# Kernel tuning notes

Measured on AMD Instinct MI355X. Metric: run time of the kernel, lower is better.

Reference implementation:

```python
import jax, jax.numpy as jnp
import numpy as np

N_NODES = 50000
N_EDGES = 1600000
IN_FEAT = 128
OUT_FEAT = 32
N_HEADS = 4
NEG_SLOPE = 0.2


def setup_inputs() -> dict:
    key = jax.random.key(0)
    ks = jax.random.split(key, 7)
    h = jax.random.normal(ks[0], (N_NODES, IN_FEAT), dtype=jnp.float32)
    W = jax.random.normal(ks[1], (IN_FEAT, N_HEADS * OUT_FEAT), dtype=jnp.float32) * 0.05
    attn_l = jax.random.normal(ks[2], (N_HEADS, OUT_FEAT), dtype=jnp.float32) * 0.1
    attn_r = jax.random.normal(ks[3], (N_HEADS, OUT_FEAT), dtype=jnp.float32) * 0.1
    bias = jax.random.normal(ks[4], (N_HEADS * OUT_FEAT,), dtype=jnp.float32) * 0.01
    src = jax.random.randint(ks[5], (N_EDGES,), 0, N_NODES, dtype=jnp.int32)
    dst = jax.random.randint(ks[6], (N_EDGES,), 0, N_NODES, dtype=jnp.int32)
    return {"h": h, "W": W, "attn_l": attn_l, "attn_r": attn_r, "bias": bias, "src": src, "dst": dst}


def reference(h, W, attn_l, attn_r, bias, src, dst):
    N = h.shape[0]
    H, F = attn_l.shape
    # linear projection, [N, H, F]
    feat = (h @ W).reshape(N, H, F)
    # per-node attention halves
    el = jnp.einsum('nhf,hf->nh', feat, attn_l)  # [N, H]
    er = jnp.einsum('nhf,hf->nh', feat, attn_r)  # [N, H]
    # edge scores: e_ij = leaky_relu(el[src] + er[dst])
    e = jax.nn.leaky_relu(el[src] + er[dst], negative_slope=NEG_SLOPE)  # [E, H]
    # edge softmax over incoming edges of each dst node (numerically stable)
    m = jax.ops.segment_max(e, dst, num_segments=N)  # [N, H]
    m = jnp.where(jnp.isfinite(m), m, jnp.zeros_like(m))  # zero-in-degree guard
    ex = jnp.exp(e - m[dst])  # [E, H]
    denom = jax.ops.segment_sum(ex, dst, num_segments=N)  # [N, H]
    alpha = ex / jnp.maximum(denom[dst], 1e-9)  # [E, H]
    # weighted scatter-sum aggregation
    msg = feat[src] * alpha[:, :, None]  # [E, H, F]
    rst = jax.ops.segment_sum(msg, dst, num_segments=N)  # [N, H, F]
    rst = rst + bias.reshape(1, H, F)
    rst = jax.nn.relu(rst)
    # wrapper: norm=None, dropout=0.0 (eval), mean over heads
    return jnp.mean(rst, axis=1)  # [N, F]
```

## Files before the change

kernel.cpp:

```cpp
#include <hip/hip_runtime.h>
#include <hip/hip_bf16.h>
#include <hip/hip_fp16.h>
#include <math.h>


#define NEG_SLOPE 0.2f
#define HEADS 4
#define FEAT_OUT 32
#define FEAT_ALL 128
#define IN_FEAT 128
#define KP 136
#define NBLK1 512
#define NBKT_MAX 512
#define CHE_MAX 3200
#define CHB_MAX 6144

typedef _Float16 half8 __attribute__((ext_vector_type(8)));
typedef float float4v __attribute__((ext_vector_type(4)));
typedef unsigned int uint4v __attribute__((ext_vector_type(4)));

__device__ __forceinline__ float leaky(float v) {
    return v > 0.f ? v : NEG_SLOPE * v;
}

__global__ __launch_bounds__(256) void k1_fused(
    const int* __restrict__ src, const int* __restrict__ dst, int E,
    int che, int nbkt,
    unsigned int* __restrict__ ds, int* __restrict__ hist,
    const float* __restrict__ h, const float* __restrict__ W,
    const float* __restrict__ attn_l, const float* __restrict__ attn_r,
    unsigned char* __restrict__ feat8, float2* __restrict__ elsc,
    float* __restrict__ er, int N, int nG) {
    __shared__ _Float16 sf[64 * KP];
    const int t = threadIdx.x;

    if ((int)blockIdx.x >= nG) {
        const int blk = blockIdx.x - nG;
        int* hb = (int*)sf;
        for (int i = t; i < nbkt; i += 256) hb[i] = 0;
        __syncthreads();
        const int e_lo = blk * che;
        int e_hi = e_lo + che; if (e_hi > E) e_hi = E;
        for (int e0 = e_lo + t * 4; e0 < e_hi; e0 += 1024) {
            if (e0 + 3 < e_hi) {
                uint4v s4 = *(const uint4v*)(src + e0);
                uint4v d4 = *(const uint4v*)(dst + e0);
                uint4v r;
#pragma unroll
                for (int j = 0; j < 4; j++) r[j] = (s4[j] << 16) | d4[j];
                *(uint4v*)(ds + e0) = r;
#pragma unroll
                for (int j = 0; j < 4; j++) atomicAdd(&hb[d4[j] >> 7], 1);
            } else {
                for (int e = e0; e < e_hi; ++e) {
                    unsigned s = (unsigned)src[e], d = (unsigned)dst[e];
                    ds[e] = (s << 16) | d;
                    atomicAdd(&hb[d >> 7], 1);
                }
            }
        }
        __syncthreads();
        for (int i = t; i < nbkt; i += 256) hist[i * NBLK1 + blk] = hb[i];
        return;
    }

    const int n0 = blockIdx.x * 64;
    const int wv_ = t >> 6;
    const int lane = t & 63;
    const int m16 = lane & 15;
    const int quad = lane >> 4;
    const int rowA = wv_ * 16 + m16;
    int nA = n0 + rowA; if (nA > N - 1) nA = N - 1;
    const float* hp = h + (size_t)nA * IN_FEAT + quad * 8;

    float4v acc[8];
#pragma unroll
    for (int i = 0; i < 8; i++) acc[i] = (float4v){0.f, 0.f, 0.f, 0.f};

#pragma unroll
    for (int k0 = 0; k0 < 128; k0 += 32) {
        float4 a0 = *(const float4*)(hp + k0);
        float4 a1 = *(const float4*)(hp + k0 + 4);
        half8 a;
        a[0] = (_Float16)a0.x; a[1] = (_Float16)a0.y;
        a[2] = (_Float16)a0.z; a[3] = (_Float16)a0.w;
        a[4] = (_Float16)a1.x; a[5] = (_Float16)a1.y;
        a[6] = (_Float16)a1.z; a[7] = (_Float16)a1.w;
        const float* wp = W + (size_t)(k0 + quad * 8) * FEAT_ALL + m16;
#pragma unroll
        for (int tN = 0; tN < 8; tN++) {
            const float* wpt = wp + tN * 16;
            half8 b;
            b[0] = (_Float16)wpt[0];
            b[1] = (_Float16)wpt[FEAT_ALL];
            b[2] = (_Float16)wpt[2 * FEAT_ALL];
            b[3] = (_Float16)wpt[3 * FEAT_ALL];
            b[4] = (_Float16)wpt[4 * FEAT_ALL];
            b[5] = (_Float16)wpt[5 * FEAT_ALL];
            b[6] = (_Float16)wpt[6 * FEAT_ALL];
            b[7] = (_Float16)wpt[7 * FEAT_ALL];
            acc[tN] = __builtin_amdgcn_mfma_f32_16x16x32_f16(a, b, acc[tN], 0, 0, 0);
        }
    }

#pragma unroll
    for (int tN = 0; tN < 8; tN++)
#pragma unroll
        for (int r = 0; r < 4; r++) {
            int row = wv_ * 16 + quad * 4 + r;
            sf[row * KP + tN * 16 + m16] = (_Float16)acc[tN][r];
        }
    __syncthreads();

    {
        int r = t >> 2, hh = t & 3;
        int n = n0 + r;
        if (n < N) {
            const _Float16* sp_ = &sf[r * KP + hh * FEAT_OUT];
            float sl = 0.f, sr = 0.f, mx = 0.f;
#pragma unroll
            for (int f = 0; f < FEAT_OUT; f++) {
                float v = (float)sp_[f];
                sl += v * attn_l[hh * FEAT_OUT + f];
                sr += v * attn_r[hh * FEAT_OUT + f];
                mx = fmaxf(mx, fabsf(v));
            }
            er[n * HEADS + hh] = sr;
            elsc[n * HEADS + hh] = make_float2(sl, mx * (1.f / 127.f));
            const float inv = mx > 0.f ? 127.f / mx : 0.f;
            unsigned int w[8];
#pragma unroll
            for (int k2 = 0; k2 < 8; k2++) {
                unsigned int wv = 0;
#pragma unroll
                for (int j = 0; j < 4; j++) {
                    float v = (float)sp_[k2 * 4 + j];
                    int q = __float2int_rn(v * inv);
                    wv |= ((unsigned int)(q & 0xff)) << (8 * j);
                }
                w[k2] = wv;
            }
            uint4* dp = (uint4*)(feat8 + (size_t)n * FEAT_ALL + hh * 32);
            dp[0] = make_uint4(w[0], w[1], w[2], w[3]);
            dp[1] = make_uint4(w[4], w[5], w[6], w[7]);
        }
    }
}

__global__ __launch_bounds__(256) void s1_scan(
    const int* __restrict__ hist, int* __restrict__ base1,
    int* __restrict__ tot, int nbkt) {
    __shared__ int sm[256];
    const int b = blockIdx.x;
    const int t = threadIdx.x;
    const int v0 = hist[b * NBLK1 + 2 * t];
    const int v1 = hist[b * NBLK1 + 2 * t + 1];
    const int s = v0 + v1;
    sm[t] = s; __syncthreads();
    for (int off = 1; off < 256; off <<= 1) {
        int x = (t >= off) ? sm[t - off] : 0;
        __syncthreads();
        sm[t] += x;
        __syncthreads();
    }
    const int excl = sm[t] - s;
    base1[(2 * t) * nbkt + b] = excl;
    base1[(2 * t + 1) * nbkt + b] = excl + v0;
    if (t == 255) tot[b] = sm[255];
}

__global__ __launch_bounds__(256) void s2_scan(
    const int* __restrict__ tot, int* __restrict__ bb, int nbkt) {
    __shared__ int sm[256];
    const int t = threadIdx.x;
    const int v0 = (2 * t < nbkt) ? tot[2 * t] : 0;
    const int v1 = (2 * t + 1 < nbkt) ? tot[2 * t + 1] : 0;
    const int s = v0 + v1;
    sm[t] = s; __syncthreads();
    for (int off = 1; off < 256; off <<= 1) {
        int x = (t >= off) ? sm[t - off] : 0;
        __syncthreads();
        sm[t] += x;
        __syncthreads();
    }
    const int excl = sm[t] - s;
    if (2 * t <= nbkt) bb[2 * t] = excl;
    if (2 * t + 1 <= nbkt) bb[2 * t + 1] = excl + v0;
}

__global__ __launch_bounds__(256) void p2_place(
    const unsigned int* __restrict__ ds, const int* __restrict__ hist,
    const int* __restrict__ base1, const int* __restrict__ bb,
    unsigned int* __restrict__ srt, int E, int che, int nbkt) {
    __shared__ int cur[NBKT_MAX];
    __shared__ int l0[NBKT_MAX];
    __shared__ int gst[NBKT_MAX];
    __shared__ int sm[256];
    __shared__ unsigned int stage[CHE_MAX];
    __shared__ int gaddr[CHE_MAX];
    const int t = threadIdx.x;
    const int blk = blockIdx.x;
    const int e_lo = blk * che;
    int e_hi = e_lo + che; if (e_hi > E) e_hi = E;
    int cnt = e_hi - e_lo; if (cnt < 0) cnt = 0;

    if (che <= CHE_MAX) {
        const int b0 = 2 * t, b1 = 2 * t + 1;
        const int h0 = (b0 < nbkt) ? hist[b0 * NBLK1 + blk] : 0;
        const int h1 = (b1 < nbkt) ? hist[b1 * NBLK1 + blk] : 0;
        const int s = h0 + h1;
        sm[t] = s; __syncthreads();
        for (int off = 1; off < 256; off <<= 1) {
            int x = (t >= off) ? sm[t - off] : 0;
            __syncthreads();
            sm[t] += x;
            __syncthreads();
        }
        const int excl = sm[t] - s;
        if (b0 < nbkt) {
            l0[b0] = excl; cur[b0] = excl;
            gst[b0] = bb[b0] + base1[blk * nbkt + b0] - excl;
        }
        if (b1 < nbkt) {
            l0[b1] = excl + h0; cur[b1] = excl + h0;
            gst[b1] = bb[b1] + base1[blk * nbkt + b1] - (excl + h0);
        }
        __syncthreads();
        for (int e0 = e_lo + t * 4; e0 < e_hi; e0 += 1024) {
            if (e0 + 3 < e_hi) {
                uint4v q = *(const uint4v*)(ds + e0);
#pragma unroll
                for (int j = 0; j < 4; j++) {
                    int b = (int)(q[j] & 0xffffu) >> 7;
                    int r = atomicAdd(&cur[b], 1);
                    stage[r] = q[j];
                    gaddr[r] = gst[b] + r;
                }
            } else {
                for (int e = e0; e < e_hi; ++e) {
                    unsigned q = ds[e];
                    int b = (int)(q & 0xffffu) >> 7;
                    int r = atomicAdd(&cur[b], 1);
                    stage[r] = q;
                    gaddr[r] = gst[b] + r;
                }
            }
        }
        __syncthreads();
        for (int i = t; i < cnt; i += 256)
            srt[gaddr[i]] = stage[i];
    } else {
        for (int i = t; i < nbkt; i += 256)
            cur[i] = bb[i] + base1[blk * nbkt + i];
        __syncthreads();
        for (int e0 = e_lo + t * 4; e0 < e_hi; e0 += 1024) {
            for (int e = e0; e < e_hi && e < e0 + 4; ++e) {
                unsigned q = ds[e];
                int b = (int)(q & 0xffffu) >> 7;
                int idx = atomicAdd(&cur[b], 1);
                srt[idx] = q;
            }
        }
    }
}

__global__ __launch_bounds__(256) void p3_bucket(
    const unsigned int* __restrict__ srt, const int* __restrict__ bb,
    unsigned short* __restrict__ slots16, unsigned int* __restrict__ rpd,
    int N) {
    __shared__ int h2[128];
    __shared__ int nbuf[128];
    __shared__ unsigned short stage16[CHB_MAX];
    const int b = blockIdx.x;
    const int t = threadIdx.x;
    const int s0 = bb[b];
    const int M = bb[b + 1] - s0;
    const int lo = b << 7;
    if (t < 128) h2[t] = 0;
    __syncthreads();
    for (int i = t; i < M; i += 256) {
        unsigned q = srt[s0 + i];
        atomicAdd(&h2[(int)(q & 0xffffu) - lo], 1);
    }
    __syncthreads();
    int hv = 0;
    if (t < 128) hv = h2[t];
    for (int off = 1; off < 128; off <<= 1) {
        int x = 0;
        if (t < 128 && t >= off) x = h2[t - off];
        __syncthreads();
        if (t < 128) h2[t] += x;
        __syncthreads();
    }
    if (t < 128) {
        const int excl = h2[t] - hv;
        nbuf[t] = excl;
        const int n = lo + t;
        if (n < N) {
            int dg = hv > 255 ? 255 : hv;
            rpd[n] = ((unsigned)(s0 + excl) << 8) | (unsigned)dg;
        }
    }
    __syncthreads();
    if (t < 128) h2[t] = nbuf[t];
    __syncthreads();
    if (M <= CHB_MAX) {
        for (int i = t; i < M; i += 256) {
            unsigned q = srt[s0 + i];
            int n7 = (int)(q & 0xffffu) - lo;
            int r = atomicAdd(&h2[n7], 1);
            stage16[r] = (unsigned short)(q >> 16);
        }
        __syncthreads();
        for (int i = t; i < M; i += 256)
            slots16[s0 + i] = stage16[i];
    } else {
        for (int i = t; i < M; i += 256) {
            unsigned q = srt[s0 + i];
            int n7 = (int)(q & 0xffffu) - lo;
            int r = atomicAdd(&h2[n7], 1);
            slots16[s0 + r] = (unsigned short)(q >> 16);
        }
    }
}

__global__ __launch_bounds__(256) void k5_node(
    const unsigned int* __restrict__ rpd, const unsigned short* __restrict__ slots16,
    const float2* __restrict__ elsc, const float* __restrict__ er,
    const unsigned char* __restrict__ feat8, const float* __restrict__ bias,
    float* __restrict__ out, int N) {
    const int lane = threadIdx.x & 63;
    const int p = blockIdx.x & 7;
    const int g = blockIdx.x >> 3;
    const int NPER = (N + 7) >> 3;
    const int hi = ((p + 1) * NPER < N) ? (p + 1) * NPER : N;
    const int n = p * NPER + g * 4 + (threadIdx.x >> 6);
    if (n >= hi) return;
    const unsigned rd = rpd[n];
    const int deg = (int)(rd & 0xffu);
    const unsigned short* sp = slots16 + (rd >> 8);

    const int sub4 = lane >> 4;
    const int q4 = lane & 15;
    const int hh = q4 >> 2;
    const float ernh = er[n * HEADS + hh];

    float acc[8];
#pragma unroll
    for (int j = 0; j < 8; j++) acc[j] = 0.f;
    float den = 0.f;

#pragma unroll 4
    for (int i = sub4; i < deg; i += 4) {
        int s = (int)sp[i];
        float2 es = elsc[s * HEADS + hh];
        float ex = __expf(leaky(es.x + ernh));
        uint2 u = *(const uint2*)(feat8 + (size_t)s * FEAT_ALL + q4 * 8);
        float exs = ex * es.y;
        den += ex;
        union { uint2 v; signed char b[8]; } cv;
        cv.v = u;
        acc[0] += exs * (float)cv.b[0];
        acc[1] += exs * (float)cv.b[1];
        acc[2] += exs * (float)cv.b[2];
        acc[3] += exs * (float)cv.b[3];
        acc[4] += exs * (float)cv.b[4];
        acc[5] += exs * (float)cv.b[5];
        acc[6] += exs * (float)cv.b[6];
        acc[7] += exs * (float)cv.b[7];
    }

#pragma unroll
    for (int j = 0; j < 8; j++) {
        acc[j] += __shfl_xor(acc[j], 16);
        acc[j] += __shfl_xor(acc[j], 32);
    }
    den += __shfl_xor(den, 16);
    den += __shfl_xor(den, 32);
    const float idh = 1.f / fmaxf(den, 1e-9f);

    const float4 b0 = ((const float4*)bias)[q4 * 2];
    const float4 b1 = ((const float4*)bias)[q4 * 2 + 1];
    float v[8];
    v[0] = fmaxf(acc[0] * idh + b0.x, 0.f); v[1] = fmaxf(acc[1] * idh + b0.y, 0.f);
    v[2] = fmaxf(acc[2] * idh + b0.z, 0.f); v[3] = fmaxf(acc[3] * idh + b0.w, 0.f);
    v[4] = fmaxf(acc[4] * idh + b1.x, 0.f); v[5] = fmaxf(acc[5] * idh + b1.y, 0.f);
    v[6] = fmaxf(acc[6] * idh + b1.z, 0.f); v[7] = fmaxf(acc[7] * idh + b1.w, 0.f);
#pragma unroll
    for (int j = 0; j < 8; j++) {
        v[j] += __shfl_xor(v[j], 4);
        v[j] += __shfl_xor(v[j], 8);
    }
    if (lane < 4) {
        float4 o0 = make_float4(v[0] * 0.25f, v[1] * 0.25f, v[2] * 0.25f, v[3] * 0.25f);
        float4 o1 = make_float4(v[4] * 0.25f, v[5] * 0.25f, v[6] * 0.25f, v[7] * 0.25f);
        float* op = out + (size_t)n * FEAT_OUT + lane * 8;
        ((float4*)op)[0] = o0;
        ((float4*)op)[1] = o1;
    }
}

extern "C" void kernel_launch(void* const* d_in, const int* in_sizes, int n_in,
                              void* d_out, int out_size, void* d_ws, size_t ws_size,
                              hipStream_t stream) {
    const float* h      = (const float*)d_in[0];
    const float* W      = (const float*)d_in[1];
    const float* attn_l = (const float*)d_in[2];
    const float* attn_r = (const float*)d_in[3];
    const float* bias   = (const float*)d_in[4];
    const int*   src    = (const int*)d_in[5];
    const int*   dst    = (const int*)d_in[6];
    float* out = (float*)d_out;

    const int N = in_sizes[0] / IN_FEAT;
    const int E = in_sizes[5];
    const int nbkt = (N + 127) >> 7;
    const int che = (((E + NBLK1 - 1) / NBLK1) + 3) & ~3;

    char* w = (char*)d_ws;
    auto alloc = [&](size_t bytes) { char* r = w; w += (bytes + 255) & ~(size_t)255; return r; };
    unsigned char* feat8   = (unsigned char*)alloc((size_t)N * FEAT_ALL);
    float2*        elsc    = (float2*)alloc((size_t)N * HEADS * sizeof(float2));
    float*         er      = (float*)alloc((size_t)N * HEADS * sizeof(float));
    unsigned int*  rpd     = (unsigned int*)alloc((size_t)N * 4);
    unsigned int*  ds      = (unsigned int*)alloc((size_t)E * 4);
    unsigned int*  srt     = (unsigned int*)alloc((size_t)E * 4);
    unsigned short* slots16 = (unsigned short*)alloc((size_t)E * 2);
    int*           hist    = (int*)alloc((size_t)NBLK1 * nbkt * 4);
    int*           base1   = (int*)alloc((size_t)NBLK1 * nbkt * 4);
    int*           tot     = (int*)alloc((size_t)nbkt * 4);
    int*           bb      = (int*)alloc((size_t)(nbkt + 1) * 4);

    const int nG = (N + 63) / 64;
    k1_fused<<<nG + NBLK1, 256, 0, stream>>>(src, dst, E, che, nbkt, ds, hist,
                                             h, W, attn_l, attn_r,
                                             feat8, elsc, er, N, nG);
    s1_scan<<<nbkt, 256, 0, stream>>>(hist, base1, tot, nbkt);
    s2_scan<<<1, 256, 0, stream>>>(tot, bb, nbkt);
    p2_place<<<NBLK1, 256, 0, stream>>>(ds, hist, base1, bb, srt, E, che, nbkt);
    p3_bucket<<<nbkt, 256, 0, stream>>>(srt, bb, slots16, rpd, N);

    const int NPER = (N + 7) >> 3;
    const int nb5 = 8 * ((NPER + 3) / 4);
    k5_node<<<nb5, 256, 0, stream>>>(rpd, slots16, elsc, er, feat8, bias, out, N);
}
```

Measured before the change: 177.6 us.

## Merge scan, place and bucket kernels into one cooperative kernel with grid syncs

Replaces four separate launches (two scans, global placement, per-bucket sort) with a single cooperative kernel of 512 blocks that separates the phases with grid.sync(). Shared memory is overlaid through a union so one block can serve every phase. The aim is to remove per-launch overhead and the gaps between dependent small kernels. In exchange, grid-wide barriers are costly, all 512 blocks must be co-resident, and phases that use only nbkt blocks leave the rest idle.

```diff
diff --git a/kernel.cpp b/kernel.cpp
--- a/kernel.cpp
+++ b/kernel.cpp
@@ -1,4 +1,5 @@
 #include <hip/hip_runtime.h>
+#include <hip/hip_cooperative_groups.h>
 #include <hip/hip_bf16.h>
 #include <hip/hip_fp16.h>
 #include <math.h>
@@ -14,6 +15,8 @@
 #define NBKT_MAX 512
 #define CHE_MAX 3200
 #define CHB_MAX 6144
+
+namespace cg = cooperative_groups;
 
 typedef _Float16 half8 __attribute__((ext_vector_type(8)));
 typedef float float4v __attribute__((ext_vector_type(4)));
@@ -147,179 +150,172 @@
     }
 }
 
-__global__ __launch_bounds__(256) void s1_scan(
-    const int* __restrict__ hist, int* __restrict__ base1,
-    int* __restrict__ tot, int nbkt) {
-    __shared__ int sm[256];
-    const int b = blockIdx.x;
-    const int t = threadIdx.x;
-    const int v0 = hist[b * NBLK1 + 2 * t];
-    const int v1 = hist[b * NBLK1 + 2 * t + 1];
-    const int s = v0 + v1;
-    sm[t] = s; __syncthreads();
-    for (int off = 1; off < 256; off <<= 1) {
-        int x = (t >= off) ? sm[t - off] : 0;
-        __syncthreads();
-        sm[t] += x;
-        __syncthreads();
-    }
-    const int excl = sm[t] - s;
-    base1[(2 * t) * nbkt + b] = excl;
-    base1[(2 * t + 1) * nbkt + b] = excl + v0;
-    if (t == 255) tot[b] = sm[255];
-}
-
-__global__ __launch_bounds__(256) void s2_scan(
-    const int* __restrict__ tot, int* __restrict__ bb, int nbkt) {
-    __shared__ int sm[256];
-    const int t = threadIdx.x;
-    const int v0 = (2 * t < nbkt) ? tot[2 * t] : 0;
-    const int v1 = (2 * t + 1 < nbkt) ? tot[2 * t + 1] : 0;
-    const int s = v0 + v1;
-    sm[t] = s; __syncthreads();
-    for (int off = 1; off < 256; off <<= 1) {
-        int x = (t >= off) ? sm[t - off] : 0;
-        __syncthreads();
-        sm[t] += x;
-        __syncthreads();
-    }
-    const int excl = sm[t] - s;
-    if (2 * t <= nbkt) bb[2 * t] = excl;
-    if (2 * t + 1 <= nbkt) bb[2 * t + 1] = excl + v0;
-}
-
-__global__ __launch_bounds__(256) void p2_place(
+__global__ __launch_bounds__(256) void ksort(
     const unsigned int* __restrict__ ds, const int* __restrict__ hist,
-    const int* __restrict__ base1, const int* __restrict__ bb,
-    unsigned int* __restrict__ srt, int E, int che, int nbkt) {
-    __shared__ int cur[NBKT_MAX];
-    __shared__ int l0[NBKT_MAX];
-    __shared__ int gst[NBKT_MAX];
-    __shared__ int sm[256];
-    __shared__ unsigned int stage[CHE_MAX];
-    __shared__ int gaddr[CHE_MAX];
+    int* __restrict__ base1, int* __restrict__ bb, int* __restrict__ tot,
+    unsigned int* __restrict__ srt, unsigned short* __restrict__ slots16,
+    unsigned int* __restrict__ rpd, int E, int che, int nbkt, int N) {
+    __shared__ union {
+        struct { int sm[256]; } a;
+        struct {
+            int cur[NBKT_MAX]; int gst[NBKT_MAX]; int sm[256];
+            unsigned int stage[CHE_MAX]; int gaddr[CHE_MAX];
+        } c;
+        struct { int h2[128]; int nbuf[128]; unsigned short stage16[CHB_MAX]; } d;
+    } u;
     const int t = threadIdx.x;
     const int blk = blockIdx.x;
-    const int e_lo = blk * che;
-    int e_hi = e_lo + che; if (e_hi > E) e_hi = E;
-    int cnt = e_hi - e_lo; if (cnt < 0) cnt = 0;
-
-    if (che <= CHE_MAX) {
-        const int b0 = 2 * t, b1 = 2 * t + 1;
-        const int h0 = (b0 < nbkt) ? hist[b0 * NBLK1 + blk] : 0;
-        const int h1 = (b1 < nbkt) ? hist[b1 * NBLK1 + blk] : 0;
-        const int s = h0 + h1;
-        sm[t] = s; __syncthreads();
+    cg::grid_group grid = cg::this_grid();
+
+    if (blk < nbkt) {
+        const int b = blk;
+        const int v0 = hist[b * NBLK1 + 2 * t];
+        const int v1 = hist[b * NBLK1 + 2 * t + 1];
+        const int s = v0 + v1;
+        u.a.sm[t] = s; __syncthreads();
         for (int off = 1; off < 256; off <<= 1) {
-            int x = (t >= off) ? sm[t - off] : 0;
-            __syncthreads();
-            sm[t] += x;
-            __syncthreads();
-        }
-        const int excl = sm[t] - s;
-        if (b0 < nbkt) {
-            l0[b0] = excl; cur[b0] = excl;
-            gst[b0] = bb[b0] + base1[blk * nbkt + b0] - excl;
-        }
-        if (b1 < nbkt) {
-            l0[b1] = excl + h0; cur[b1] = excl + h0;
-            gst[b1] = bb[b1] + base1[blk * nbkt + b1] - (excl + h0);
-        }
-        __syncthreads();
-        for (int e0 = e_lo + t * 4; e0 < e_hi; e0 += 1024) {
-            if (e0 + 3 < e_hi) {
-                uint4v q = *(const uint4v*)(ds + e0);
-#pragma unroll
-                for (int j = 0; j < 4; j++) {
-                    int b = (int)(q[j] & 0xffffu) >> 7;
-                    int r = atomicAdd(&cur[b], 1);
-                    stage[r] = q[j];
-                    gaddr[r] = gst[b] + r;
+            int x = (t >= off) ? u.a.sm[t - off] : 0;
+            __syncthreads();
+            u.a.sm[t] += x;
+            __syncthreads();
+        }
+        const int excl = u.a.sm[t] - s;
+        base1[(2 * t) * nbkt + b] = excl;
+        base1[(2 * t + 1) * nbkt + b] = excl + v0;
+        if (t == 255) tot[b] = u.a.sm[255];
+    }
+    grid.sync();
+
+    if (blk == 0) {
+        const int v0 = (2 * t < nbkt) ? tot[2 * t] : 0;
+        const int v1 = (2 * t + 1 < nbkt) ? tot[2 * t + 1] : 0;
+        const int s = v0 + v1;
+        u.a.sm[t] = s; __syncthreads();
+        for (int off = 1; off < 256; off <<= 1) {
+            int x = (t >= off) ? u.a.sm[t - off] : 0;
+            __syncthreads();
+            u.a.sm[t] += x;
+            __syncthreads();
+        }
+        const int excl = u.a.sm[t] - s;
+        if (2 * t <= nbkt) bb[2 * t] = excl;
+        if (2 * t + 1 <= nbkt) bb[2 * t + 1] = excl + v0;
+    }
+    grid.sync();
+
+    {
+        const int e_lo = blk * che;
+        int e_hi = e_lo + che; if (e_hi > E) e_hi = E;
+        int cnt = e_hi - e_lo; if (cnt < 0) cnt = 0;
+        if (che <= CHE_MAX) {
+            const int b0 = 2 * t, b1 = 2 * t + 1;
+            const int h0 = (b0 < nbkt) ? hist[b0 * NBLK1 + blk] : 0;
+            const int h1 = (b1 < nbkt) ? hist[b1 * NBLK1 + blk] : 0;
+            const int s = h0 + h1;
+            u.c.sm[t] = s; __syncthreads();
+            for (int off = 1; off < 256; off <<= 1) {
+                int x = (t >= off) ? u.c.sm[t - off] : 0;
+                __syncthreads();
+                u.c.sm[t] += x;
+                __syncthreads();
+            }
+            const int excl = u.c.sm[t] - s;
+            if (b0 < nbkt) {
+                u.c.cur[b0] = excl;
+                u.c.gst[b0] = bb[b0] + base1[blk * nbkt + b0] - excl;
+            }
+            if (b1 < nbkt) {
+                u.c.cur[b1] = excl + h0;
+                u.c.gst[b1] = bb[b1] + base1[blk * nbkt + b1] - (excl + h0);
+            }
+            __syncthreads();
+            for (int e0 = e_lo + t * 4; e0 < e_hi; e0 += 1024) {
+                if (e0 + 3 < e_hi) {
+                    uint4v q = *(const uint4v*)(ds + e0);
+#pragma unroll
+                    for (int j = 0; j < 4; j++) {
+                        int b = (int)(q[j] & 0xffffu) >> 7;
+                        int r = atomicAdd(&u.c.cur[b], 1);
+                        u.c.stage[r] = q[j];
+                        u.c.gaddr[r] = u.c.gst[b] + r;
+                    }
+                } else {
+                    for (int e = e0; e < e_hi; ++e) {
+                        unsigned q = ds[e];
+                        int b = (int)(q & 0xffffu) >> 7;
+                        int r = atomicAdd(&u.c.cur[b], 1);
+                        u.c.stage[r] = q;
+                        u.c.gaddr[r] = u.c.gst[b] + r;
+                    }
                 }
-            } else {
-                for (int e = e0; e < e_hi; ++e) {
-                    unsigned q = ds[e];
-                    int b = (int)(q & 0xffffu) >> 7;
-                    int r = atomicAdd(&cur[b], 1);
-                    stage[r] = q;
-                    gaddr[r] = gst[b] + r;
-                }
-            }
-        }
-        __syncthreads();
-        for (int i = t; i < cnt; i += 256)
-            srt[gaddr[i]] = stage[i];
-    } else {
-        for (int i = t; i < nbkt; i += 256)
-            cur[i] = bb[i] + base1[blk * nbkt + i];
-        __syncthreads();
-        for (int e0 = e_lo + t * 4; e0 < e_hi; e0 += 1024) {
-            for (int e = e0; e < e_hi && e < e0 + 4; ++e) {
+            }
+            __syncthreads();
+            for (int i = t; i < cnt; i += 256)
+                srt[u.c.gaddr[i]] = u.c.stage[i];
+        } else {
+            for (int i = t; i < nbkt; i += 256)
+                u.c.cur[i] = bb[i] + base1[blk * nbkt + i];
+            __syncthreads();
+            for (int e = e_lo + t; e < e_hi; e += 256) {
                 unsigned q = ds[e];
                 int b = (int)(q & 0xffffu) >> 7;
-                int idx = atomicAdd(&cur[b], 1);
+                int idx = atomicAdd(&u.c.cur[b], 1);
                 srt[idx] = q;
             }
         }
     }
-}
-
-__global__ __launch_bounds__(256) void p3_bucket(
-    const unsigned int* __restrict__ srt, const int* __restrict__ bb,
-    unsigned short* __restrict__ slots16, unsigned int* __restrict__ rpd,
-    int N) {
-    __shared__ int h2[128];
-    __shared__ int nbuf[128];
-    __shared__ unsigned short stage16[CHB_MAX];
-    const int b = blockIdx.x;
-    const int t = threadIdx.x;
-    const int s0 = bb[b];
-    const int M = bb[b + 1] - s0;
-    const int lo = b << 7;
-    if (t < 128) h2[t] = 0;
-    __syncthreads();
-    for (int i = t; i < M; i += 256) {
-        unsigned q = srt[s0 + i];
-        atomicAdd(&h2[(int)(q & 0xffffu) - lo], 1);
-    }
-    __syncthreads();
-    int hv = 0;
-    if (t < 128) hv = h2[t];
-    for (int off = 1; off < 128; off <<= 1) {
-        int x = 0;
-        if (t < 128 && t >= off) x = h2[t - off];
-        __syncthreads();
-        if (t < 128) h2[t] += x;
-        __syncthreads();
-    }
-    if (t < 128) {
-        const int excl = h2[t] - hv;
-        nbuf[t] = excl;
-        const int n = lo + t;
-        if (n < N) {
-            int dg = hv > 255 ? 255 : hv;
-            rpd[n] = ((unsigned)(s0 + excl) << 8) | (unsigned)dg;
-        }
-    }
-    __syncthreads();
-    if (t < 128) h2[t] = nbuf[t];
-    __syncthreads();
-    if (M <= CHB_MAX) {
+    grid.sync();
+
+    if (blk < nbkt) {
+        const int b = blk;
+        const int s0 = bb[b];
+        const int M = bb[b + 1] - s0;
+        const int lo = b << 7;
+        if (t < 128) u.d.h2[t] = 0;
+        __syncthreads();
         for (int i = t; i < M; i += 256) {
             unsigned q = srt[s0 + i];
-            int n7 = (int)(q & 0xffffu) - lo;
-            int r = atomicAdd(&h2[n7], 1);
-            stage16[r] = (unsigned short)(q >> 16);
-        }
-        __syncthreads();
-        for (int i = t; i < M; i += 256)
-            slots16[s0 + i] = stage16[i];
-    } else {
-        for (int i = t; i < M; i += 256) {
-            unsigned q = srt[s0 + i];
-            int n7 = (int)(q & 0xffffu) - lo;
-            int r = atomicAdd(&h2[n7], 1);
-            slots16[s0 + r] = (unsigned short)(q >> 16);
+            atomicAdd(&u.d.h2[(int)(q & 0xffffu) - lo], 1);
+        }
+        __syncthreads();
+        int hv = 0;
+        if (t < 128) hv = u.d.h2[t];
+        for (int off = 1; off < 128; off <<= 1) {
+            int x = 0;
+            if (t < 128 && t >= off) x = u.d.h2[t - off];
+            __syncthreads();
+            if (t < 128) u.d.h2[t] += x;
+            __syncthreads();
+        }
+        if (t < 128) {
+            const int excl = u.d.h2[t] - hv;
+            u.d.nbuf[t] = excl;
+            const int n = lo + t;
+            if (n < N) {
+                int dg = hv > 255 ? 255 : hv;
+                rpd[n] = ((unsigned)(s0 + excl) << 8) | (unsigned)dg;
+            }
+        }
+        __syncthreads();
+        if (t < 128) u.d.h2[t] = u.d.nbuf[t];
+        __syncthreads();
+        if (M <= CHB_MAX) {
+            for (int i = t; i < M; i += 256) {
+                unsigned q = srt[s0 + i];
+                int n7 = (int)(q & 0xffffu) - lo;
+                int r = atomicAdd(&u.d.h2[n7], 1);
+                u.d.stage16[r] = (unsigned short)(q >> 16);
+            }
+            __syncthreads();
+            for (int i = t; i < M; i += 256)
+                slots16[s0 + i] = u.d.stage16[i];
+        } else {
+            for (int i = t; i < M; i += 256) {
+                unsigned q = srt[s0 + i];
+                int n7 = (int)(q & 0xffffu) - lo;
+                int r = atomicAdd(&u.d.h2[n7], 1);
+                slots16[s0 + r] = (unsigned short)(q >> 16);
+            }
         }
     }
 }
@@ -413,9 +409,9 @@
     float* out = (float*)d_out;
 
     const int N = in_sizes[0] / IN_FEAT;
-    const int E = in_sizes[5];
-    const int nbkt = (N + 127) >> 7;
-    const int che = (((E + NBLK1 - 1) / NBLK1) + 3) & ~3;
+    int E = in_sizes[5];
+    int nbkt = (N + 127) >> 7;
+    int che = (((E + NBLK1 - 1) / NBLK1) + 3) & ~3;
 
     char* w = (char*)d_ws;
     auto alloc = [&](size_t bytes) { char* r = w; w += (bytes + 255) & ~(size_t)255; return r; };
@@ -430,15 +426,17 @@
     int*           base1   = (int*)alloc((size_t)NBLK1 * nbkt * 4);
     int*           tot     = (int*)alloc((size_t)nbkt * 4);
     int*           bb      = (int*)alloc((size_t)(nbkt + 1) * 4);
+    int N_ = N;
 
     const int nG = (N + 63) / 64;
     k1_fused<<<nG + NBLK1, 256, 0, stream>>>(src, dst, E, che, nbkt, ds, hist,
                                              h, W, attn_l, attn_r,
                                              feat8, elsc, er, N, nG);
-    s1_scan<<<nbkt, 256, 0, stream>>>(hist, base1, tot, nbkt);
-    s2_scan<<<1, 256, 0, stream>>>(tot, bb, nbkt);
-    p2_place<<<NBLK1, 256, 0, stream>>>(ds, hist, base1, bb, srt, E, che, nbkt);
-    p3_bucket<<<nbkt, 256, 0, stream>>>(srt, bb, slots16, rpd, N);
+
+    void* args[] = {(void*)&ds, (void*)&hist, (void*)&base1, (void*)&bb,
+                    (void*)&tot, (void*)&srt, (void*)&slots16, (void*)&rpd,
+                    (void*)&E, (void*)&che, (void*)&nbkt, (void*)&N_};
+    hipLaunchCooperativeKernel((void*)ksort, dim3(NBLK1), dim3(256), args, 0, stream);
 
     const int NPER = (N + 7) >> 3;
     const int nb5 = 8 * ((NPER + 3) / 4);
```

After: 385.3 us. 117% more time.

## Fuse bucket-level sort into aggregation kernel and fold total scan into placement

Applied to the files above, without the earlier changes.

Removes the separate total-scan kernel by having every p2_place block redundantly scan the bucket totals in shared memory. Removes the p3_bucket kernel and the rpd/slots16 buffers: the aggregation kernel now handles a quarter-bucket of 32 nodes per block, counting-sorts that quarter's edges into shared memory, and aggregates straight from there. This cuts two launches and one global write/read pass over the edges. In exchange, each bucket's edge list is scanned four times (once per quarter), each block recomputes its start offset with a reduction, and there is a slow fallback path when a quarter holds more than the staging capacity.

```diff
diff --git a/kernel.cpp b/kernel.cpp
--- a/kernel.cpp
+++ b/kernel.cpp
@@ -13,7 +13,7 @@
 #define NBLK1 512
 #define NBKT_MAX 512
 #define CHE_MAX 3200
-#define CHB_MAX 6144
+#define QCAP 2048
 
 typedef _Float16 half8 __attribute__((ext_vector_type(8)));
 typedef float float4v __attribute__((ext_vector_type(4)));
@@ -169,32 +169,13 @@
     if (t == 255) tot[b] = sm[255];
 }
 
-__global__ __launch_bounds__(256) void s2_scan(
-    const int* __restrict__ tot, int* __restrict__ bb, int nbkt) {
-    __shared__ int sm[256];
-    const int t = threadIdx.x;
-    const int v0 = (2 * t < nbkt) ? tot[2 * t] : 0;
-    const int v1 = (2 * t + 1 < nbkt) ? tot[2 * t + 1] : 0;
-    const int s = v0 + v1;
-    sm[t] = s; __syncthreads();
-    for (int off = 1; off < 256; off <<= 1) {
-        int x = (t >= off) ? sm[t - off] : 0;
-        __syncthreads();
-        sm[t] += x;
-        __syncthreads();
-    }
-    const int excl = sm[t] - s;
-    if (2 * t <= nbkt) bb[2 * t] = excl;
-    if (2 * t + 1 <= nbkt) bb[2 * t + 1] = excl + v0;
-}
-
 __global__ __launch_bounds__(256) void p2_place(
     const unsigned int* __restrict__ ds, const int* __restrict__ hist,
-    const int* __restrict__ base1, const int* __restrict__ bb,
+    const int* __restrict__ base1, const int* __restrict__ tot,
     unsigned int* __restrict__ srt, int E, int che, int nbkt) {
     __shared__ int cur[NBKT_MAX];
-    __shared__ int l0[NBKT_MAX];
     __shared__ int gst[NBKT_MAX];
+    __shared__ int bbloc[NBKT_MAX];
     __shared__ int sm[256];
     __shared__ unsigned int stage[CHE_MAX];
     __shared__ int gaddr[CHE_MAX];
@@ -203,6 +184,23 @@
     const int e_lo = blk * che;
     int e_hi = e_lo + che; if (e_hi > E) e_hi = E;
     int cnt = e_hi - e_lo; if (cnt < 0) cnt = 0;
+
+    {
+        const int v0 = (2 * t < nbkt) ? tot[2 * t] : 0;
+        const int v1 = (2 * t + 1 < nbkt) ? tot[2 * t + 1] : 0;
+        const int s = v0 + v1;
+        sm[t] = s; __syncthreads();
+        for (int off = 1; off < 256; off <<= 1) {
+            int x = (t >= off) ? sm[t - off] : 0;
+            __syncthreads();
+            sm[t] += x;
+            __syncthreads();
+        }
+        const int excl = sm[t] - s;
+        if (2 * t < nbkt) bbloc[2 * t] = excl;
+        if (2 * t + 1 < nbkt) bbloc[2 * t + 1] = excl + v0;
+    }
+    __syncthreads();
 
     if (che <= CHE_MAX) {
         const int b0 = 2 * t, b1 = 2 * t + 1;
@@ -218,12 +216,12 @@
         }
         const int excl = sm[t] - s;
         if (b0 < nbkt) {
-            l0[b0] = excl; cur[b0] = excl;
-            gst[b0] = bb[b0] + base1[blk * nbkt + b0] - excl;
+            cur[b0] = excl;
+            gst[b0] = bbloc[b0] + base1[blk * nbkt + b0] - excl;
         }
         if (b1 < nbkt) {
-            l0[b1] = excl + h0; cur[b1] = excl + h0;
-            gst[b1] = bb[b1] + base1[blk * nbkt + b1] - (excl + h0);
+            cur[b1] = excl + h0;
+            gst[b1] = bbloc[b1] + base1[blk * nbkt + b1] - (excl + h0);
         }
         __syncthreads();
         for (int e0 = e_lo + t * 4; e0 < e_hi; e0 += 1024) {
@@ -251,152 +249,164 @@
             srt[gaddr[i]] = stage[i];
     } else {
         for (int i = t; i < nbkt; i += 256)
-            cur[i] = bb[i] + base1[blk * nbkt + i];
-        __syncthreads();
-        for (int e0 = e_lo + t * 4; e0 < e_hi; e0 += 1024) {
-            for (int e = e0; e < e_hi && e < e0 + 4; ++e) {
-                unsigned q = ds[e];
-                int b = (int)(q & 0xffffu) >> 7;
-                int idx = atomicAdd(&cur[b], 1);
-                srt[idx] = q;
-            }
-        }
-    }
-}
-
-__global__ __launch_bounds__(256) void p3_bucket(
-    const unsigned int* __restrict__ srt, const int* __restrict__ bb,
-    unsigned short* __restrict__ slots16, unsigned int* __restrict__ rpd,
-    int N) {
-    __shared__ int h2[128];
-    __shared__ int nbuf[128];
-    __shared__ unsigned short stage16[CHB_MAX];
-    const int b = blockIdx.x;
+            cur[i] = bbloc[i] + base1[blk * nbkt + i];
+        __syncthreads();
+        for (int e = e_lo + t; e < e_hi; e += 256) {
+            unsigned q = ds[e];
+            int b = (int)(q & 0xffffu) >> 7;
+            int idx = atomicAdd(&cur[b], 1);
+            srt[idx] = q;
+        }
+    }
+}
+
+__global__ __launch_bounds__(256) void k5_bkt(
+    const unsigned int* __restrict__ srt, const int* __restrict__ tot,
+    const float2* __restrict__ elsc, const float* __restrict__ er,
+    const unsigned char* __restrict__ feat8, const float* __restrict__ bias,
+    float* __restrict__ out, int N, int nbkt) {
+    __shared__ int red[256];
+    __shared__ int rowptr[33];
+    __shared__ int curq[32];
+    __shared__ unsigned short stage16[QCAP];
     const int t = threadIdx.x;
-    const int s0 = bb[b];
-    const int M = bb[b + 1] - s0;
-    const int lo = b << 7;
-    if (t < 128) h2[t] = 0;
+    const int p = blockIdx.x & 7;
+    const int kk_ = blockIdx.x >> 3;
+    const int b = (kk_ >> 2) * 8 + p;
+    const int qtr = kk_ & 3;
+    if (b >= nbkt) return;
+
+    int partial = 0;
+    for (int i = t; i < b; i += 256) partial += tot[i];
+    red[t] = partial; __syncthreads();
+    for (int off = 128; off > 0; off >>= 1) {
+        if (t < off) red[t] += red[t + off];
+        __syncthreads();
+    }
+    const int s0 = red[0];
+    const int M = tot[b];
+    const int lo = (b << 7) + qtr * 32;
+
+    if (t < 32) curq[t] = 0;
     __syncthreads();
     for (int i = t; i < M; i += 256) {
-        unsigned q = srt[s0 + i];
-        atomicAdd(&h2[(int)(q & 0xffffu) - lo], 1);
+        int u = (int)(srt[s0 + i] & 0xffffu) - lo;
+        if ((unsigned)u < 32u) atomicAdd(&curq[u], 1);
     }
     __syncthreads();
-    int hv = 0;
-    if (t < 128) hv = h2[t];
-    for (int off = 1; off < 128; off <<= 1) {
-        int x = 0;
-        if (t < 128 && t >= off) x = h2[t - off];
-        __syncthreads();
-        if (t < 128) h2[t] += x;
-        __syncthreads();
-    }
-    if (t < 128) {
-        const int excl = h2[t] - hv;
-        nbuf[t] = excl;
-        const int n = lo + t;
-        if (n < N) {
-            int dg = hv > 255 ? 255 : hv;
-            rpd[n] = ((unsigned)(s0 + excl) << 8) | (unsigned)dg;
-        }
+    if (t == 0) {
+        int acc = 0;
+#pragma unroll
+        for (int j = 0; j < 32; j++) { rowptr[j] = acc; acc += curq[j]; }
+        rowptr[32] = acc;
     }
     __syncthreads();
-    if (t < 128) h2[t] = nbuf[t];
-    __syncthreads();
-    if (M <= CHB_MAX) {
+    const int Mq = rowptr[32];
+    const bool staged = (Mq <= QCAP);
+    if (staged) {
+        if (t < 32) curq[t] = rowptr[t];
+        __syncthreads();
         for (int i = t; i < M; i += 256) {
             unsigned q = srt[s0 + i];
-            int n7 = (int)(q & 0xffffu) - lo;
-            int r = atomicAdd(&h2[n7], 1);
-            stage16[r] = (unsigned short)(q >> 16);
-        }
-        __syncthreads();
-        for (int i = t; i < M; i += 256)
-            slots16[s0 + i] = stage16[i];
-    } else {
-        for (int i = t; i < M; i += 256) {
-            unsigned q = srt[s0 + i];
-            int n7 = (int)(q & 0xffffu) - lo;
-            int r = atomicAdd(&h2[n7], 1);
-            slots16[s0 + r] = (unsigned short)(q >> 16);
-        }
-    }
-}
-
-__global__ __launch_bounds__(256) void k5_node(
-    const unsigned int* __restrict__ rpd, const unsigned short* __restrict__ slots16,
-    const float2* __restrict__ elsc, const float* __restrict__ er,
-    const unsigned char* __restrict__ feat8, const float* __restrict__ bias,
-    float* __restrict__ out, int N) {
-    const int lane = threadIdx.x & 63;
-    const int p = blockIdx.x & 7;
-    const int g = blockIdx.x >> 3;
-    const int NPER = (N + 7) >> 3;
-    const int hi = ((p + 1) * NPER < N) ? (p + 1) * NPER : N;
-    const int n = p * NPER + g * 4 + (threadIdx.x >> 6);
-    if (n >= hi) return;
-    const unsigned rd = rpd[n];
-    const int deg = (int)(rd & 0xffu);
-    const unsigned short* sp = slots16 + (rd >> 8);
-
+            int u = (int)(q & 0xffffu) - lo;
+            if ((unsigned)u < 32u) {
+                int r = atomicAdd(&curq[u], 1);
+                stage16[r] = (unsigned short)(q >> 16);
+            }
+        }
+        __syncthreads();
+    }
+
+    const int lane = t & 63;
+    const int wv = t >> 6;
     const int sub4 = lane >> 4;
     const int q4 = lane & 15;
     const int hh = q4 >> 2;
-    const float ernh = er[n * HEADS + hh];
-
-    float acc[8];
-#pragma unroll
-    for (int j = 0; j < 8; j++) acc[j] = 0.f;
-    float den = 0.f;
-
+    const float4 b0v = ((const float4*)bias)[q4 * 2];
+    const float4 b1v = ((const float4*)bias)[q4 * 2 + 1];
+
+    for (int kk = 0; kk < 8; kk++) {
+        const int u = wv * 8 + kk;
+        const int n = lo + u;
+        if (n >= N) continue;
+        const int rp = rowptr[u];
+        const int deg = rowptr[u + 1] - rp;
+        const float ernh = er[n * HEADS + hh];
+
+        float acc[8];
+#pragma unroll
+        for (int j = 0; j < 8; j++) acc[j] = 0.f;
+        float den = 0.f;
+
+        if (staged) {
 #pragma unroll 4
-    for (int i = sub4; i < deg; i += 4) {
-        int s = (int)sp[i];
-        float2 es = elsc[s * HEADS + hh];
-        float ex = __expf(leaky(es.x + ernh));
-        uint2 u = *(const uint2*)(feat8 + (size_t)s * FEAT_ALL + q4 * 8);
-        float exs = ex * es.y;
-        den += ex;
-        union { uint2 v; signed char b[8]; } cv;
-        cv.v = u;
-        acc[0] += exs * (float)cv.b[0];
-        acc[1] += exs * (float)cv.b[1];
-        acc[2] += exs * (float)cv.b[2];
-        acc[3] += exs * (float)cv.b[3];
-        acc[4] += exs * (float)cv.b[4];
-        acc[5] += exs * (float)cv.b[5];
-        acc[6] += exs * (float)cv.b[6];
-        acc[7] += exs * (float)cv.b[7];
-    }
-
-#pragma unroll
-    for (int j = 0; j < 8; j++) {
-        acc[j] += __shfl_xor(acc[j], 16);
-        acc[j] += __shfl_xor(acc[j], 32);
-    }
-    den += __shfl_xor(den, 16);
-    den += __shfl_xor(den, 32);
-    const float idh = 1.f / fmaxf(den, 1e-9f);
-
-    const float4 b0 = ((const float4*)bias)[q4 * 2];
-    const float4 b1 = ((const float4*)bias)[q4 * 2 + 1];
-    float v[8];
-    v[0] = fmaxf(acc[0] * idh + b0.x, 0.f); v[1] = fmaxf(acc[1] * idh + b0.y, 0.f);
-    v[2] = fmaxf(acc[2] * idh + b0.z, 0.f); v[3] = fmaxf(acc[3] * idh + b0.w, 0.f);
-    v[4] = fmaxf(acc[4] * idh + b1.x, 0.f); v[5] = fmaxf(acc[5] * idh + b1.y, 0.f);
-    v[6] = fmaxf(acc[6] * idh + b1.z, 0.f); v[7] = fmaxf(acc[7] * idh + b1.w, 0.f);
-#pragma unroll
-    for (int j = 0; j < 8; j++) {
-        v[j] += __shfl_xor(v[j], 4);
-        v[j] += __shfl_xor(v[j], 8);
-    }
-    if (lane < 4) {
-        float4 o0 = make_float4(v[0] * 0.25f, v[1] * 0.25f, v[2] * 0.25f, v[3] * 0.25f);
-        float4 o1 = make_float4(v[4] * 0.25f, v[5] * 0.25f, v[6] * 0.25f, v[7] * 0.25f);
-        float* op = out + (size_t)n * FEAT_OUT + lane * 8;
-        ((float4*)op)[0] = o0;
-        ((float4*)op)[1] = o1;
+            for (int i = sub4; i < deg; i += 4) {
+                int s = (int)stage16[rp + i];
+                float2 es = elsc[s * HEADS + hh];
+                float ex = __expf(leaky(es.x + ernh));
+                uint2 uv = *(const uint2*)(feat8 + (size_t)s * FEAT_ALL + q4 * 8);
+                float exs = ex * es.y;
+                den += ex;
+                union { uint2 v; signed char c[8]; } cv;
+                cv.v = uv;
+                acc[0] += exs * (float)cv.c[0];
+                acc[1] += exs * (float)cv.c[1];
+                acc[2] += exs * (float)cv.c[2];
+                acc[3] += exs * (float)cv.c[3];
+                acc[4] += exs * (float)cv.c[4];
+                acc[5] += exs * (float)cv.c[5];
+                acc[6] += exs * (float)cv.c[6];
+                acc[7] += exs * (float)cv.c[7];
+            }
+        } else {
+            for (int i = sub4; i < M; i += 4) {
+                unsigned q = srt[s0 + i];
+                if ((int)(q & 0xffffu) != n) continue;
+                int s = (int)(q >> 16);
+                float2 es = elsc[s * HEADS + hh];
+                float ex = __expf(leaky(es.x + ernh));
+                uint2 uv = *(const uint2*)(feat8 + (size_t)s * FEAT_ALL + q4 * 8);
+                float exs = ex * es.y;
+                den += ex;
+                union { uint2 v; signed char c[8]; } cv;
+                cv.v = uv;
+                acc[0] += exs * (float)cv.c[0];
+                acc[1] += exs * (float)cv.c[1];
+                acc[2] += exs * (float)cv.c[2];
+                acc[3] += exs * (float)cv.c[3];
+                acc[4] += exs * (float)cv.c[4];
+                acc[5] += exs * (float)cv.c[5];
+                acc[6] += exs * (float)cv.c[6];
+                acc[7] += exs * (float)cv.c[7];
+            }
+        }
+
+#pragma unroll
+        for (int j = 0; j < 8; j++) {
+            acc[j] += __shfl_xor(acc[j], 16);
+            acc[j] += __shfl_xor(acc[j], 32);
+        }
+        den += __shfl_xor(den, 16);
+        den += __shfl_xor(den, 32);
+        const float idh = 1.f / fmaxf(den, 1e-9f);
+
+        float v[8];
+        v[0] = fmaxf(acc[0] * idh + b0v.x, 0.f); v[1] = fmaxf(acc[1] * idh + b0v.y, 0.f);
+        v[2] = fmaxf(acc[2] * idh + b0v.z, 0.f); v[3] = fmaxf(acc[3] * idh + b0v.w, 0.f);
+        v[4] = fmaxf(acc[4] * idh + b1v.x, 0.f); v[5] = fmaxf(acc[5] * idh + b1v.y, 0.f);
+        v[6] = fmaxf(acc[6] * idh + b1v.z, 0.f); v[7] = fmaxf(acc[7] * idh + b1v.w, 0.f);
+#pragma unroll
+        for (int j = 0; j < 8; j++) {
+            v[j] += __shfl_xor(v[j], 4);
+            v[j] += __shfl_xor(v[j], 8);
+        }
+        if (lane < 4) {
+            float4 o0 = make_float4(v[0] * 0.25f, v[1] * 0.25f, v[2] * 0.25f, v[3] * 0.25f);
+            float4 o1 = make_float4(v[4] * 0.25f, v[5] * 0.25f, v[6] * 0.25f, v[7] * 0.25f);
+            float* op = out + (size_t)n * FEAT_OUT + lane * 8;
+            ((float4*)op)[0] = o0;
+            ((float4*)op)[1] = o1;
+        }
     }
 }
 
@@ -422,25 +432,19 @@
     unsigned char* feat8   = (unsigned char*)alloc((size_t)N * FEAT_ALL);
     float2*        elsc    = (float2*)alloc((size_t)N * HEADS * sizeof(float2));
     float*         er      = (float*)alloc((size_t)N * HEADS * sizeof(float));
-    unsigned int*  rpd     = (unsigned int*)alloc((size_t)N * 4);
     unsigned int*  ds      = (unsigned int*)alloc((size_t)E * 4);
     unsigned int*  srt     = (unsigned int*)alloc((size_t)E * 4);
-    unsigned short* slots16 = (unsigned short*)alloc((size_t)E * 2);
     int*           hist    = (int*)alloc((size_t)NBLK1 * nbkt * 4);
     int*           base1   = (int*)alloc((size_t)NBLK1 * nbkt * 4);
     int*           tot     = (int*)alloc((size_t)nbkt * 4);
-    int*           bb      = (int*)alloc((size_t)(nbkt + 1) * 4);
 
     const int nG = (N + 63) / 64;
     k1_fused<<<nG + NBLK1, 256, 0, stream>>>(src, dst, E, che, nbkt, ds, hist,
                                              h, W, attn_l, attn_r,
                                              feat8, elsc, er, N, nG);
     s1_scan<<<nbkt, 256, 0, stream>>>(hist, base1, tot, nbkt);
-    s2_scan<<<1, 256, 0, stream>>>(tot, bb, nbkt);
-    p2_place<<<NBLK1, 256, 0, stream>>>(ds, hist, base1, bb, srt, E, che, nbkt);
-    p3_bucket<<<nbkt, 256, 0, stream>>>(srt, bb, slots16, rpd, N);
-
-    const int NPER = (N + 7) >> 3;
-    const int nb5 = 8 * ((NPER + 3) / 4);
-    k5_node<<<nb5, 256, 0, stream>>>(rpd, slots16, elsc, er, feat8, bias, out, N);
-}
+    p2_place<<<NBLK1, 256, 0, stream>>>(ds, hist, base1, tot, srt, E, che, nbkt);
+
+    const int nqb = 8 * (((nbkt + 7) / 8) * 4);
+    k5_bkt<<<nqb, 256, 0, stream>>>(srt, tot, elsc, er, feat8, bias, out, N, nbkt);
+}
```

Measured after the change: 189.2 us. 6.5% more time.

## Fold bucket-offset scan into consumers and precompute per-edge attention weights once

Applied to the files above, without the earlier changes.

The single-block s2_scan kernel is removed. p2_place now recomputes the bucket prefix scan of tot in every block, and p3_bucket derives its start offset with a block reduction, which saves one kernel launch. In k5_node, each wave first computes exp/leaky scores once per edge and head into shared memory along with the source indices. The feature aggregation loop then reads those instead of having 16 lanes per edge redo the exp and the elsc gather. This adds redundant scan work per block, extra shared memory, and a __syncthreads, and k5 lanes no longer exit early.

```diff
diff --git a/kernel.cpp b/kernel.cpp
--- a/kernel.cpp
+++ b/kernel.cpp
@@ -169,32 +169,13 @@
     if (t == 255) tot[b] = sm[255];
 }
 
-__global__ __launch_bounds__(256) void s2_scan(
-    const int* __restrict__ tot, int* __restrict__ bb, int nbkt) {
-    __shared__ int sm[256];
-    const int t = threadIdx.x;
-    const int v0 = (2 * t < nbkt) ? tot[2 * t] : 0;
-    const int v1 = (2 * t + 1 < nbkt) ? tot[2 * t + 1] : 0;
-    const int s = v0 + v1;
-    sm[t] = s; __syncthreads();
-    for (int off = 1; off < 256; off <<= 1) {
-        int x = (t >= off) ? sm[t - off] : 0;
-        __syncthreads();
-        sm[t] += x;
-        __syncthreads();
-    }
-    const int excl = sm[t] - s;
-    if (2 * t <= nbkt) bb[2 * t] = excl;
-    if (2 * t + 1 <= nbkt) bb[2 * t + 1] = excl + v0;
-}
-
 __global__ __launch_bounds__(256) void p2_place(
     const unsigned int* __restrict__ ds, const int* __restrict__ hist,
-    const int* __restrict__ base1, const int* __restrict__ bb,
+    const int* __restrict__ base1, const int* __restrict__ tot,
     unsigned int* __restrict__ srt, int E, int che, int nbkt) {
     __shared__ int cur[NBKT_MAX];
-    __shared__ int l0[NBKT_MAX];
     __shared__ int gst[NBKT_MAX];
+    __shared__ int bbloc[NBKT_MAX];
     __shared__ int sm[256];
     __shared__ unsigned int stage[CHE_MAX];
     __shared__ int gaddr[CHE_MAX];
@@ -203,6 +184,23 @@
     const int e_lo = blk * che;
     int e_hi = e_lo + che; if (e_hi > E) e_hi = E;
     int cnt = e_hi - e_lo; if (cnt < 0) cnt = 0;
+
+    {
+        const int v0 = (2 * t < nbkt) ? tot[2 * t] : 0;
+        const int v1 = (2 * t + 1 < nbkt) ? tot[2 * t + 1] : 0;
+        const int s = v0 + v1;
+        sm[t] = s; __syncthreads();
+        for (int off = 1; off < 256; off <<= 1) {
+            int x = (t >= off) ? sm[t - off] : 0;
+            __syncthreads();
+            sm[t] += x;
+            __syncthreads();
+        }
+        const int excl = sm[t] - s;
+        if (2 * t < nbkt) bbloc[2 * t] = excl;
+        if (2 * t + 1 < nbkt) bbloc[2 * t + 1] = excl + v0;
+    }
+    __syncthreads();
 
     if (che <= CHE_MAX) {
         const int b0 = 2 * t, b1 = 2 * t + 1;
@@ -218,12 +216,12 @@
         }
         const int excl = sm[t] - s;
         if (b0 < nbkt) {
-            l0[b0] = excl; cur[b0] = excl;
-            gst[b0] = bb[b0] + base1[blk * nbkt + b0] - excl;
+            cur[b0] = excl;
+            gst[b0] = bbloc[b0] + base1[blk * nbkt + b0] - excl;
         }
         if (b1 < nbkt) {
-            l0[b1] = excl + h0; cur[b1] = excl + h0;
-            gst[b1] = bb[b1] + base1[blk * nbkt + b1] - (excl + h0);
+            cur[b1] = excl + h0;
+            gst[b1] = bbloc[b1] + base1[blk * nbkt + b1] - (excl + h0);
         }
         __syncthreads();
         for (int e0 = e_lo + t * 4; e0 < e_hi; e0 += 1024) {
@@ -251,30 +249,36 @@
             srt[gaddr[i]] = stage[i];
     } else {
         for (int i = t; i < nbkt; i += 256)
-            cur[i] = bb[i] + base1[blk * nbkt + i];
-        __syncthreads();
-        for (int e0 = e_lo + t * 4; e0 < e_hi; e0 += 1024) {
-            for (int e = e0; e < e_hi && e < e0 + 4; ++e) {
-                unsigned q = ds[e];
-                int b = (int)(q & 0xffffu) >> 7;
-                int idx = atomicAdd(&cur[b], 1);
-                srt[idx] = q;
-            }
+            cur[i] = bbloc[i] + base1[blk * nbkt + i];
+        __syncthreads();
+        for (int e = e_lo + t; e < e_hi; e += 256) {
+            unsigned q = ds[e];
+            int b = (int)(q & 0xffffu) >> 7;
+            int idx = atomicAdd(&cur[b], 1);
+            srt[idx] = q;
         }
     }
 }
 
 __global__ __launch_bounds__(256) void p3_bucket(
-    const unsigned int* __restrict__ srt, const int* __restrict__ bb,
+    const unsigned int* __restrict__ srt, const int* __restrict__ tot,
     unsigned short* __restrict__ slots16, unsigned int* __restrict__ rpd,
-    int N) {
+    int N, int nbkt) {
+    __shared__ int red[256];
     __shared__ int h2[128];
     __shared__ int nbuf[128];
     __shared__ unsigned short stage16[CHB_MAX];
     const int b = blockIdx.x;
     const int t = threadIdx.x;
-    const int s0 = bb[b];
-    const int M = bb[b + 1] - s0;
+    int partial = 0;
+    for (int i = t; i < b; i += 256) partial += tot[i];
+    red[t] = partial; __syncthreads();
+    for (int off = 128; off > 0; off >>= 1) {
+        if (t < off) red[t] += red[t + off];
+        __syncthreads();
+    }
+    const int s0 = red[0];
+    const int M = tot[b];
     const int lo = b << 7;
     if (t < 128) h2[t] = 0;
     __syncthreads();
@@ -329,45 +333,68 @@
     const float2* __restrict__ elsc, const float* __restrict__ er,
     const unsigned char* __restrict__ feat8, const float* __restrict__ bias,
     float* __restrict__ out, int N) {
-    const int lane = threadIdx.x & 63;
+    __shared__ float exbuf[4][1024];
+    __shared__ unsigned short sldb[4][256];
+    const int t = threadIdx.x;
+    const int lane = t & 63;
+    const int wv = t >> 6;
     const int p = blockIdx.x & 7;
     const int g = blockIdx.x >> 3;
     const int NPER = (N + 7) >> 3;
     const int hi = ((p + 1) * NPER < N) ? (p + 1) * NPER : N;
-    const int n = p * NPER + g * 4 + (threadIdx.x >> 6);
-    if (n >= hi) return;
-    const unsigned rd = rpd[n];
+    const int n = p * NPER + g * 4 + wv;
+    const bool valid = (n < hi);
+    const unsigned rd = valid ? rpd[n] : 0u;
     const int deg = (int)(rd & 0xffu);
     const unsigned short* sp = slots16 + (rd >> 8);
+    float* exw = exbuf[wv];
+    unsigned short* slw = sldb[wv];
+
+    const int e4 = lane >> 2;
+    const int hd = lane & 3;
+    const float ern = valid ? er[n * HEADS + hd] : 0.f;
+    float den = 0.f;
+    for (int i0 = 0; i0 < deg; i0 += 16) {
+        const int i = i0 + e4;
+        if (i < deg) {
+            const int s = (int)sp[i];
+            const float2 es = elsc[s * HEADS + hd];
+            const float ex = __expf(leaky(es.x + ern));
+            exw[i * 4 + hd] = ex * es.y;
+            if (hd == 0) slw[i] = (unsigned short)s;
+            den += ex;
+        }
+    }
+    den += __shfl_xor(den, 4);
+    den += __shfl_xor(den, 8);
+    den += __shfl_xor(den, 16);
+    den += __shfl_xor(den, 32);
+    __syncthreads();
 
     const int sub4 = lane >> 4;
     const int q4 = lane & 15;
     const int hh = q4 >> 2;
-    const float ernh = er[n * HEADS + hh];
+    const unsigned char* fb = feat8 + q4 * 8;
 
     float acc[8];
 #pragma unroll
     for (int j = 0; j < 8; j++) acc[j] = 0.f;
-    float den = 0.f;
 
 #pragma unroll 4
     for (int i = sub4; i < deg; i += 4) {
-        int s = (int)sp[i];
-        float2 es = elsc[s * HEADS + hh];
-        float ex = __expf(leaky(es.x + ernh));
-        uint2 u = *(const uint2*)(feat8 + (size_t)s * FEAT_ALL + q4 * 8);
-        float exs = ex * es.y;
-        den += ex;
-        union { uint2 v; signed char b[8]; } cv;
+        const int s = (int)slw[i];
+        const float exs = exw[i * 4 + hh];
+        uint2 u = *(const uint2*)(fb + (size_t)s * FEAT_ALL);
+        union { uint2 v; signed char c[8]; } cv;
         cv.v = u;
-        acc[0] += exs * (float)cv.b[0];
-        acc[1] += exs * (float)cv.b[1];
-        acc[2] += exs * (float)cv.b[2];
-        acc[3] += exs * (float)cv.b[3];
-        acc[4] += exs * (float)cv.b[4];
-        acc[5] += exs * (float)cv.b[5];
-        acc[6] += exs * (float)cv.b[6];
-        acc[7] += exs * (float)cv.b[7];
+        acc[0] += exs * (float)cv.c[0];
+        acc[1] += exs * (float)cv.c[1];
+        acc[2] += exs * (float)cv.c[2];
+        acc[3] += exs * (float)cv.c[3];
+        acc[4] += exs * (float)cv.c[4];
+        acc[5] += exs * (float)cv.c[5];
+        acc[6] += exs * (float)cv.c[6];
+        acc[7] += exs * (float)cv.c[7];
     }
 
 #pragma unroll
@@ -375,9 +402,8 @@
         acc[j] += __shfl_xor(acc[j], 16);
         acc[j] += __shfl_xor(acc[j], 32);
     }
-    den += __shfl_xor(den, 16);
-    den += __shfl_xor(den, 32);
-    const float idh = 1.f / fmaxf(den, 1e-9f);
+    const float denh = __shfl(den, hh);
+    const float idh = 1.f / fmaxf(denh, 1e-9f);
 
     const float4 b0 = ((const float4*)bias)[q4 * 2];
     const float4 b1 = ((const float4*)bias)[q4 * 2 + 1];
@@ -391,7 +417,7 @@
         v[j] += __shfl_xor(v[j], 4);
         v[j] += __shfl_xor(v[j], 8);
     }
-    if (lane < 4) {
+    if (valid && lane < 4) {
         float4 o0 = make_float4(v[0] * 0.25f, v[1] * 0.25f, v[2] * 0.25f, v[3] * 0.25f);
         float4 o1 = make_float4(v[4] * 0.25f, v[5] * 0.25f, v[6] * 0.25f, v[7] * 0.25f);
         float* op = out + (size_t)n * FEAT_OUT + lane * 8;
@@ -429,16 +455,14 @@
     int*           hist    = (int*)alloc((size_t)NBLK1 * nbkt * 4);
     int*           base1   = (int*)alloc((size_t)NBLK1 * nbkt * 4);
     int*           tot     = (int*)alloc((size_t)nbkt * 4);
-    int*           bb      = (int*)alloc((size_t)(nbkt + 1) * 4);
 
     const int nG = (N + 63) / 64;
     k1_fused<<<nG + NBLK1, 256, 0, stream>>>(src, dst, E, che, nbkt, ds, hist,
                                              h, W, attn_l, attn_r,
                                              feat8, elsc, er, N, nG);
     s1_scan<<<nbkt, 256, 0, stream>>>(hist, base1, tot, nbkt);
-    s2_scan<<<1, 256, 0, stream>>>(tot, bb, nbkt);
-    p2_place<<<NBLK1, 256, 0, stream>>>(ds, hist, base1, bb, srt, E, che, nbkt);
-    p3_bucket<<<nbkt, 256, 0, stream>>>(srt, bb, slots16, rpd, N);
+    p2_place<<<NBLK1, 256, 0, stream>>>(ds, hist, base1, tot, srt, E, che, nbkt);
+    p3_bucket<<<nbkt, 256, 0, stream>>>(srt, tot, slots16, rpd, N, nbkt);
 
     const int NPER = (N + 7) >> 3;
     const int nb5 = 8 * ((NPER + 3) / 4);
```

Result: no change. 177.8 us (+0.1%).
